# Kernel tuning notes

Measured on AMD Instinct MI355X. Metric: run time of the kernel, lower is better.

Reference implementation:

```python
import jax, jax.numpy as jnp
import numpy as np

# RosaAttention config constants
H = 16       # num_rosa_heads
KV = 4       # num_rosa_key_value_heads
QKB = 64     # num_rosa_query_key_bits
VB = 64      # num_rosa_value_bits
HID = 2048   # hidden_size
TAU = 1.0    # temperature buffer


def setup_inputs() -> dict:
    key = jax.random.key(0)
    ks = jax.random.split(key, 8)
    B, S = 2, 2048
    sc = 0.02
    return {
        "x": jax.random.normal(ks[0], (B, S, HID), jnp.float32),
        "attention_mask": jnp.ones((B, S), jnp.int32),
        "Wq": jax.random.normal(ks[1], (HID, H * QKB), jnp.float32) * sc,
        "Wk": jax.random.normal(ks[2], (HID, KV * QKB), jnp.float32) * sc,
        "Wv": jax.random.normal(ks[3], (HID, KV * VB), jnp.float32) * sc,
        "Wo": jax.random.normal(ks[4], (H * VB, HID), jnp.float32) * sc,
        "emb0": jnp.full((H, VB), -1e-05, jnp.float32),
        "emb1": jnp.full((H, VB), +1e-05, jnp.float32),
    }


def reference(x, attention_mask, Wq, Wk, Wv, Wo, emb0, emb1):
    B, S, _ = x.shape
    rep = H // KV
    # projections -> [b, s, heads, bits]
    xq = (x @ Wq).reshape(B, S, H, QKB)
    xk = (x @ Wk).reshape(B, S, KV, QKB)
    xv = (x @ Wv).reshape(B, S, KV, VB)
    # repeat_kv: each kv head repeated n_rep times contiguously
    xk = jnp.repeat(xk, rep, axis=2)   # [b, s, H, QKB]
    xv = jnp.repeat(xv, rep, axis=2)   # [b, s, H, VB]
    # soft bit quantization of q/k, tau-scaled bit-similarity score
    qb = jnp.tanh(xq)
    kb = jnp.tanh(xk)
    scores = jnp.einsum('bqhd,bkhd->bhqk', qb, kb) / (TAU * QKB)
    # causal mask + padding mask (mask True = attend)
    causal = jnp.tril(jnp.ones((S, S), bool))
    mask = causal[None, None] & attention_mask.astype(bool)[:, None, None, :]
    scores = jnp.where(mask, scores, jnp.finfo(scores.dtype).min)
    probs = jax.nn.softmax(scores, axis=-1)        # [b, h, q, k]
    # soft-binarized values: per-bit probabilities, attended, then mapped
    # through learned per-head bit embeddings emb0 (bit=0) / emb1 (bit=1)
    vp = jax.nn.sigmoid(xv)                        # [b, s, H, VB]
    ctx = jnp.einsum('bhqk,bkhv->bqhv', probs, vp) # [b, s, H, VB]
    out_bits = ctx * emb1[None, None] + (1.0 - ctx) * emb0[None, None]
    out = out_bits.reshape(B, S, H * VB) @ Wo      # [b, s, HID]
    return out
```

## Files before the change

kernel.cpp:

```cpp
#include <hip/hip_runtime.h>
#include <math.h>

typedef short bf16x8 __attribute__((ext_vector_type(8)));
typedef float f32x4 __attribute__((ext_vector_type(4)));

#define MFMA_BF16(A,B,C) __builtin_amdgcn_mfma_f32_16x16x32_bf16(A,B,C,0,0,0)

__device__ __forceinline__ unsigned short f2b(float x) {
    union { float f; unsigned int u; } v; v.f = x;
    unsigned int r = v.u + 0x7FFFu + ((v.u >> 16) & 1u);
    return (unsigned short)(r >> 16);
}

__device__ __forceinline__ void gload16(const unsigned short* g, unsigned short* l) {
    __builtin_amdgcn_global_load_lds(
        (const __attribute__((address_space(1))) unsigned int*)(g),
        (__attribute__((address_space(3))) unsigned int*)(l),
        16, 0, 0);
}

__global__ __launch_bounds__(256) void conv_bf16(const float* __restrict__ s,
                                                 unsigned short* __restrict__ d, int n)
{
    int i = blockIdx.x * blockDim.x + threadIdx.x;
    int stride = gridDim.x * blockDim.x;
    for (int idx = i * 4; idx < n; idx += stride * 4) {
        float4 v = *(const float4*)(s + idx);
        ushort4 o;
        o.x = f2b(v.x); o.y = f2b(v.y); o.z = f2b(v.z); o.w = f2b(v.w);
        *(ushort4*)(d + idx) = o;
    }
}

__global__ __launch_bounds__(256) void transp_conv_qkv(const float* __restrict__ Wq,
                                                       const float* __restrict__ Wk,
                                                       const float* __restrict__ Wv,
                                                       unsigned short* __restrict__ dst)
{
    __shared__ float t[32][33];
    const int tx = threadIdx.x, ty = threadIdx.y;
    int bx = blockIdx.x;
    const float* src; int C, cb, dco;
    if (bx < 32)      { src = Wq; C = 1024; cb = bx;      dco = 0; }
    else if (bx < 40) { src = Wk; C = 256;  cb = bx - 32; dco = 1024; }
    else              { src = Wv; C = 256;  cb = bx - 40; dco = 1280; }
    const int c = cb * 32 + tx;
    const int r0 = blockIdx.y * 32;
#pragma unroll
    for (int i = 0; i < 4; ++i)
        t[ty + i * 8][tx] = src[(size_t)(r0 + ty + i * 8) * C + c];
    __syncthreads();
    const int cc = cb * 32 + ty;
#pragma unroll
    for (int i = 0; i < 4; ++i)
        dst[(size_t)(dco + cc + i * 8) * 2048 + r0 + tx] = f2b(t[tx][ty + i * 8]);
}

__global__ __launch_bounds__(256) void transp_conv(const float* __restrict__ src, int R, int C,
                                                   unsigned short* __restrict__ dst, int pitch)
{
    __shared__ float t[32][33];
    const int tx = threadIdx.x, ty = threadIdx.y;
    const int c = blockIdx.x * 32 + tx;
    const int r0 = blockIdx.y * 32;
#pragma unroll
    for (int i = 0; i < 4; ++i)
        t[ty + i * 8][tx] = src[(size_t)(r0 + ty + i * 8) * C + c];
    __syncthreads();
    const int cc = blockIdx.x * 32 + ty;
#pragma unroll
    for (int i = 0; i < 4; ++i)
        dst[(size_t)(cc + i * 8) * pitch + r0 + tx] = f2b(t[tx][ty + i * 8]);
}

template <int MODE>
__global__ __launch_bounds__(256, 3) void gemm_bt_mfma(
    const unsigned short* __restrict__ A,
    const unsigned short* __restrict__ Bt,
    int M, int N, int K,
    float* __restrict__ Cf,
    unsigned short* __restrict__ qh,
    unsigned short* __restrict__ kh,
    unsigned short* __restrict__ vtt)
{
    __shared__ __align__(16) unsigned short As[2][2 * 128 * 32];
    __shared__ __align__(16) unsigned short Bs[2][2 * 64 * 32];

    const int tid = threadIdx.x;
    const int w = tid >> 6, lane = tid & 63, l15 = lane & 15, quad = lane >> 4;
    const int wm = w & 1, wn = w >> 1;
    const int m0 = blockIdx.y * 128, n0 = blockIdx.x * 64;

    f32x4 acc[4][2];
    const f32x4 zero4 = {0.f, 0.f, 0.f, 0.f};
#pragma unroll
    for (int i = 0; i < 4; ++i)
#pragma unroll
        for (int j = 0; j < 2; ++j) acc[i][j] = zero4;

    const int lrow = lane >> 2, lcol = (lane & 3) * 8;
    const unsigned short* AgL = A  + (size_t)(m0 + w * 32 + lrow) * K + lcol;
    const unsigned short* BgL = Bt + (size_t)(n0 + w * 16 + lrow) * K + lcol;

#pragma unroll
    for (int t = 0; t < 4; ++t) {
        const int sub = t >> 1, half = t & 1;
        gload16(AgL + (size_t)(half * 16) * K + sub * 32,
                &As[0][sub * 4096 + (w * 32 + half * 16) * 32]);
    }
#pragma unroll
    for (int kk = 0; kk < 2; ++kk)
        gload16(BgL + kk * 32, &Bs[0][kk * 2048 + (w * 16) * 32]);
    __syncthreads();

    int cb = 0;
    for (int k0 = 0; k0 < K; k0 += 64) {
        if (k0 + 64 < K) {
            const int nb = cb ^ 1;
#pragma unroll
            for (int t = 0; t < 4; ++t) {
                const int sub = t >> 1, half = t & 1;
                gload16(AgL + (size_t)(half * 16) * K + (k0 + 64) + sub * 32,
                        &As[nb][sub * 4096 + (w * 32 + half * 16) * 32]);
            }
#pragma unroll
            for (int kk = 0; kk < 2; ++kk)
                gload16(BgL + (k0 + 64) + kk * 32, &Bs[nb][kk * 2048 + (w * 16) * 32]);
        }

        bf16x8 af[4][2], bf[2][2];
#pragma unroll
        for (int kk = 0; kk < 2; ++kk) {
#pragma unroll
            for (int mt = 0; mt < 4; ++mt)
                af[mt][kk] = *(const bf16x8*)&As[cb][kk * 4096 + (wm * 64 + mt * 16 + l15) * 32 + quad * 8];
#pragma unroll
            for (int nt = 0; nt < 2; ++nt)
                bf[nt][kk] = *(const bf16x8*)&Bs[cb][kk * 2048 + (wn * 32 + nt * 16 + l15) * 32 + quad * 8];
        }
#pragma unroll
        for (int kk = 0; kk < 2; ++kk)
#pragma unroll
            for (int mt = 0; mt < 4; ++mt)
#pragma unroll
                for (int nt = 0; nt < 2; ++nt)
                    acc[mt][nt] = MFMA_BF16(af[mt][kk], bf[nt][kk], acc[mt][nt]);

        __syncthreads();
        cb ^= 1;
    }

    if (MODE == 0) {
#pragma unroll
        for (int mt = 0; mt < 4; ++mt)
#pragma unroll
            for (int nt = 0; nt < 2; ++nt) {
                const int gn = n0 + wn * 32 + nt * 16 + l15;
#pragma unroll
                for (int r = 0; r < 4; ++r) {
                    const int gm = m0 + wm * 64 + mt * 16 + quad * 4 + r;
                    Cf[(size_t)gm * N + gn] = acc[mt][nt][r];
                }
            }
    } else {
        if (n0 < 1024) {
#pragma unroll
            for (int mt = 0; mt < 4; ++mt)
#pragma unroll
                for (int nt = 0; nt < 2; ++nt) {
                    const int gn = n0 + wn * 32 + nt * 16 + l15;
#pragma unroll
                    for (int r = 0; r < 4; ++r) {
                        const int gm = m0 + wm * 64 + mt * 16 + quad * 4 + r;
                        qh[(size_t)gm * 1024 + gn] = f2b(tanhf(acc[mt][nt][r]));
                    }
                }
        } else if (n0 < 1280) {
#pragma unroll
            for (int mt = 0; mt < 4; ++mt)
#pragma unroll
                for (int nt = 0; nt < 2; ++nt) {
                    const int gn = n0 + wn * 32 + nt * 16 + l15 - 1024;
#pragma unroll
                    for (int r = 0; r < 4; ++r) {
                        const int gm = m0 + wm * 64 + mt * 16 + quad * 4 + r;
                        kh[(size_t)gm * 256 + gn] = f2b(tanhf(acc[mt][nt][r]));
                    }
                }
        } else {
#pragma unroll
            for (int mt = 0; mt < 4; ++mt)
#pragma unroll
                for (int nt = 0; nt < 2; ++nt) {
                    const int gn = n0 + wn * 32 + nt * 16 + l15 - 1280;
                    const int g = gn >> 6, vv = gn & 63;
                    const int s0 = m0 + wm * 64 + mt * 16 + quad * 4;
                    const int b = s0 >> 11, sl = s0 & 2047;
                    ushort4 pk;
                    unsigned short* pp = (unsigned short*)&pk;
#pragma unroll
                    for (int r = 0; r < 4; ++r) {
                        float sv = 1.0f / (1.0f + __expf(-acc[mt][nt][r]));
                        pp[r] = f2b(sv);
                    }
                    *(ushort4*)&vtt[((size_t)(b * 4 + g) * 64 + vv) * 2048 + sl] = pk;
                }
        }
    }
}

__global__ __launch_bounds__(256) void rosa_attn_mfma(
    const unsigned short* __restrict__ qh,
    const unsigned short* __restrict__ kh,
    const unsigned short* __restrict__ vtt,
    const int* __restrict__ amask,
    const float* __restrict__ emb0,
    const float* __restrict__ emb1,
    unsigned short* __restrict__ ob)
{
    __shared__ __align__(16) unsigned short Ks[2][64][72];
    __shared__ __align__(16) unsigned short Vs[2][64][72];
    __shared__ __align__(16) unsigned short Ps[4][16][72];
    __shared__ float Mskf[2][64];

    const int pairI = blockIdx.x;
    const int h = blockIdx.y, b = blockIdx.z, g = h >> 2;
    const int tid = threadIdx.x;
    const int w = tid >> 6, lane = tid & 63, l15 = lane & 15, quad = lane >> 4;

    const int srow0 = tid >> 3,         soff0 = (tid & 7) * 8;
    const int srow1 = (tid + 256) >> 3, soff1 = ((tid + 256) & 7) * 8;

    const unsigned short* kbase = kh + (size_t)b * 2048 * 256 + g * 64;
    const unsigned short* vbase = vtt + ((size_t)(b * 4 + g) * 64) * 2048;

    const f32x4 zero4 = {0.f, 0.f, 0.f, 0.f};
    const float cexp = 0.0225421100f;

    for (int half = 0; half < 2; ++half) {
        const int qt = (half == 0) ? pairI : 31 - pairI;
        const int q0 = qt * 64;
        const int nkt = qt + 1;
        const int qg = q0 + w * 16 + l15;

        const unsigned short* qrow = qh + ((size_t)(b * 2048 + q0 + w * 16 + l15) * 16 + h) * 64;
        const bf16x8 qf0 = *(const bf16x8*)(qrow + quad * 8);
        const bf16x8 qf1 = *(const bf16x8*)(qrow + 32 + quad * 8);

        f32x4 oacc[4];
#pragma unroll
        for (int t = 0; t < 4; ++t) oacc[t] = zero4;
        float psum = 0.0f;

        __syncthreads();
        {
            uint4 k0r = *(const uint4*)(kbase + (size_t)srow0 * 256 + soff0);
            uint4 k1r = *(const uint4*)(kbase + (size_t)srow1 * 256 + soff1);
            uint4 v0r = *(const uint4*)(vbase + (size_t)srow0 * 2048 + soff0);
            uint4 v1r = *(const uint4*)(vbase + (size_t)srow1 * 2048 + soff1);
            int mr = (tid < 64) ? amask[b * 2048 + tid] : 0;
            *(uint4*)&Ks[0][srow0][soff0] = k0r;
            *(uint4*)&Ks[0][srow1][soff1] = k1r;
            *(uint4*)&Vs[0][srow0][soff0] = v0r;
            *(uint4*)&Vs[0][srow1][soff1] = v1r;
            if (tid < 64) Mskf[0][tid] = mr ? 1.0f : 0.0f;
        }
        __syncthreads();

        int cb = 0;
        for (int kt = 0; kt < nkt; ++kt) {
            const bool haveNext = (kt + 1 < nkt);
            uint4 k0r, k1r, v0r, v1r;
            int mr = 0;
            if (haveNext) {
                const int kn = (kt + 1) * 64;
                k0r = *(const uint4*)(kbase + (size_t)(kn + srow0) * 256 + soff0);
                k1r = *(const uint4*)(kbase + (size_t)(kn + srow1) * 256 + soff1);
                v0r = *(const uint4*)(vbase + (size_t)srow0 * 2048 + kn + soff0);
                v1r = *(const uint4*)(vbase + (size_t)srow1 * 2048 + kn + soff1);
                if (tid < 64) mr = amask[b * 2048 + kn + tid];
            }

            const int k0 = kt * 64;
            const bool diag = (kt == qt);
            const int ntlim = diag ? (w + 1) : 4;

#pragma unroll
            for (int nt = 0; nt < 4; ++nt) {
                ushort4 pk;
                if (nt < ntlim) {
                    bf16x8 kf0 = *(const bf16x8*)&Ks[cb][nt * 16 + l15][quad * 8];
                    bf16x8 kf1 = *(const bf16x8*)&Ks[cb][nt * 16 + l15][32 + quad * 8];
                    f32x4 sc = MFMA_BF16(kf0, qf0, zero4);
                    sc = MFMA_BF16(kf1, qf1, sc);
                    float4 mv = *(const float4*)&Mskf[cb][nt * 16 + quad * 4];
                    const float* mvp = (const float*)&mv;
                    unsigned short* pp = (unsigned short*)&pk;
#pragma unroll
                    for (int r = 0; r < 4; ++r) {
                        float p = __builtin_exp2f(sc[r] * cexp) * mvp[r];
                        if (diag) {
                            const int jg = k0 + nt * 16 + quad * 4 + r;
                            p = (jg <= qg) ? p : 0.0f;
                        }
                        psum += p;
                        pp[r] = f2b(p);
                    }
                } else {
                    pk.x = 0; pk.y = 0; pk.z = 0; pk.w = 0;
                }
                *(ushort4*)&Ps[w][l15][nt * 16 + quad * 4] = pk;
            }

            const bf16x8 pf0 = *(const bf16x8*)&Ps[w][l15][quad * 8];
            const bf16x8 pf1 = *(const bf16x8*)&Ps[w][l15][32 + quad * 8];
#pragma unroll
            for (int nt = 0; nt < 4; ++nt) {
                bf16x8 vf0 = *(const bf16x8*)&Vs[cb][nt * 16 + l15][quad * 8];
                bf16x8 vf1 = *(const bf16x8*)&Vs[cb][nt * 16 + l15][32 + quad * 8];
                oacc[nt] = MFMA_BF16(pf0, vf0, oacc[nt]);
                oacc[nt] = MFMA_BF16(pf1, vf1, oacc[nt]);
            }

            if (haveNext) {
                const int nb = cb ^ 1;
                *(uint4*)&Ks[nb][srow0][soff0] = k0r;
                *(uint4*)&Ks[nb][srow1][soff1] = k1r;
                *(uint4*)&Vs[nb][srow0][soff0] = v0r;
                *(uint4*)&Vs[nb][srow1][soff1] = v1r;
                if (tid < 64) Mskf[nb][tid] = mr ? 1.0f : 0.0f;
                __syncthreads();
                cb = nb;
            }
        }

        float l = psum;
        l += __shfl_xor(l, 16);
        l += __shfl_xor(l, 32);
        float lq[4];
#pragma unroll
        for (int r = 0; r < 4; ++r) lq[r] = __shfl(l, quad * 4 + r);

#pragma unroll
        for (int nt = 0; nt < 4; ++nt) {
            const float e0 = emb0[h * 64 + nt * 16 + l15];
            const float e1 = emb1[h * 64 + nt * 16 + l15];
#pragma unroll
            for (int r = 0; r < 4; ++r) {
                const float ctx = oacc[nt][r] / lq[r];
                const float val = e0 + ctx * (e1 - e0);
                const size_t s_idx = (size_t)(b * 2048 + q0 + w * 16 + quad * 4 + r);
                ob[(s_idx * 16 + h) * 64 + nt * 16 + l15] = f2b(val);
            }
        }
    }
}

extern "C" void kernel_launch(void* const* d_in, const int* in_sizes, int n_in,
                              void* d_out, int out_size, void* d_ws, size_t ws_size,
                              hipStream_t stream)
{
    const float* x    = (const float*)d_in[0];
    const int*   amask= (const int*)d_in[1];
    const float* Wq   = (const float*)d_in[2];
    const float* Wk   = (const float*)d_in[3];
    const float* Wv   = (const float*)d_in[4];
    const float* Wo   = (const float*)d_in[5];
    const float* emb0 = (const float*)d_in[6];
    const float* emb1 = (const float*)d_in[7];
    float* out = (float*)d_out;

    char* base = (char*)d_ws;
    unsigned short* xh    = (unsigned short*)(base);
    unsigned short* ob    = xh;
    unsigned short* Wqkvt = (unsigned short*)(base + (16u << 20));
    unsigned short* Wot   = (unsigned short*)(base + (22u << 20));
    unsigned short* qh    = (unsigned short*)(base + (26u << 20));
    unsigned short* kh    = (unsigned short*)(base + (34u << 20));
    unsigned short* vtt   = (unsigned short*)(base + (36u << 20));

    conv_bf16<<<2048, 256, 0, stream>>>(x, xh, 4096 * 2048);
    transp_conv_qkv<<<dim3(48, 64), dim3(32, 8), 0, stream>>>(Wq, Wk, Wv, Wqkvt);
    transp_conv<<<dim3(64, 32), dim3(32, 8), 0, stream>>>(Wo, 1024, 2048, Wot, 1024);

    gemm_bt_mfma<1><<<dim3(24, 32), 256, 0, stream>>>(xh, Wqkvt, 4096, 1536, 2048,
                                                      nullptr, qh, kh, vtt);
    rosa_attn_mfma<<<dim3(16, 16, 2), 256, 0, stream>>>(qh, kh, vtt, amask, emb0, emb1, ob);
    gemm_bt_mfma<0><<<dim3(32, 32), 256, 0, stream>>>(ob, Wot, 4096, 2048, 1024,
                                                      out, nullptr, nullptr, nullptr);
}
```

Measured before the change: 238.1 us.

## Stage attention K/V tiles via direct global-to-LDS loads, one query tile per block

After: 267.6 us. 12.4% more time.

```diff
diff --git a/kernel.cpp b/kernel.cpp
--- a/kernel.cpp
+++ b/kernel.cpp
@@ -17,6 +17,12 @@
         (const __attribute__((address_space(1))) unsigned int*)(g),
         (__attribute__((address_space(3))) unsigned int*)(l),
         16, 0, 0);
+}
+__device__ __forceinline__ void gload4(const int* g, int* l) {
+    __builtin_amdgcn_global_load_lds(
+        (const __attribute__((address_space(1))) unsigned int*)(g),
+        (__attribute__((address_space(3))) unsigned int*)(l),
+        4, 0, 0);
 }
 
 __global__ __launch_bounds__(256) void conv_bf16(const float* __restrict__ s,
@@ -209,7 +215,7 @@
     }
 }
 
-__global__ __launch_bounds__(256) void rosa_attn_mfma(
+__global__ __launch_bounds__(256, 3) void rosa_attn_mfma(
     const unsigned short* __restrict__ qh,
     const unsigned short* __restrict__ kh,
     const unsigned short* __restrict__ vtt,
@@ -218,140 +224,120 @@
     const float* __restrict__ emb1,
     unsigned short* __restrict__ ob)
 {
-    __shared__ __align__(16) unsigned short Ks[2][64][72];
-    __shared__ __align__(16) unsigned short Vs[2][64][72];
+    __shared__ __align__(16) unsigned short Ks[2][2][64 * 32];
+    __shared__ __align__(16) unsigned short Vs[2][2][64 * 32];
     __shared__ __align__(16) unsigned short Ps[4][16][72];
-    __shared__ float Mskf[2][64];
-
-    const int pairI = blockIdx.x;
+    __shared__ int Mski[2][64];
+
+    const int qt = 31 - blockIdx.x;
     const int h = blockIdx.y, b = blockIdx.z, g = h >> 2;
     const int tid = threadIdx.x;
     const int w = tid >> 6, lane = tid & 63, l15 = lane & 15, quad = lane >> 4;
 
-    const int srow0 = tid >> 3,         soff0 = (tid & 7) * 8;
-    const int srow1 = (tid + 256) >> 3, soff1 = ((tid + 256) & 7) * 8;
-
+    const int q0 = qt * 64;
+    const int nkt = qt + 1;
+    const int qg = q0 + w * 16 + l15;
+
+    const int lrow = lane >> 2, lcol = (lane & 3) * 8;
     const unsigned short* kbase = kh + (size_t)b * 2048 * 256 + g * 64;
     const unsigned short* vbase = vtt + ((size_t)(b * 4 + g) * 64) * 2048;
+    const int* mbase = amask + b * 2048;
+
+    const unsigned short* qrow = qh + ((size_t)(b * 2048 + q0 + w * 16 + l15) * 16 + h) * 64;
+    const bf16x8 qf0 = *(const bf16x8*)(qrow + quad * 8);
+    const bf16x8 qf1 = *(const bf16x8*)(qrow + 32 + quad * 8);
 
     const f32x4 zero4 = {0.f, 0.f, 0.f, 0.f};
     const float cexp = 0.0225421100f;
 
-    for (int half = 0; half < 2; ++half) {
-        const int qt = (half == 0) ? pairI : 31 - pairI;
-        const int q0 = qt * 64;
-        const int nkt = qt + 1;
-        const int qg = q0 + w * 16 + l15;
-
-        const unsigned short* qrow = qh + ((size_t)(b * 2048 + q0 + w * 16 + l15) * 16 + h) * 64;
-        const bf16x8 qf0 = *(const bf16x8*)(qrow + quad * 8);
-        const bf16x8 qf1 = *(const bf16x8*)(qrow + 32 + quad * 8);
-
-        f32x4 oacc[4];
-#pragma unroll
-        for (int t = 0; t < 4; ++t) oacc[t] = zero4;
-        float psum = 0.0f;
-
-        __syncthreads();
-        {
-            uint4 k0r = *(const uint4*)(kbase + (size_t)srow0 * 256 + soff0);
-            uint4 k1r = *(const uint4*)(kbase + (size_t)srow1 * 256 + soff1);
-            uint4 v0r = *(const uint4*)(vbase + (size_t)srow0 * 2048 + soff0);
-            uint4 v1r = *(const uint4*)(vbase + (size_t)srow1 * 2048 + soff1);
-            int mr = (tid < 64) ? amask[b * 2048 + tid] : 0;
-            *(uint4*)&Ks[0][srow0][soff0] = k0r;
-            *(uint4*)&Ks[0][srow1][soff1] = k1r;
-            *(uint4*)&Vs[0][srow0][soff0] = v0r;
-            *(uint4*)&Vs[0][srow1][soff1] = v1r;
-            if (tid < 64) Mskf[0][tid] = mr ? 1.0f : 0.0f;
-        }
-        __syncthreads();
-
-        int cb = 0;
-        for (int kt = 0; kt < nkt; ++kt) {
-            const bool haveNext = (kt + 1 < nkt);
-            uint4 k0r, k1r, v0r, v1r;
-            int mr = 0;
-            if (haveNext) {
-                const int kn = (kt + 1) * 64;
-                k0r = *(const uint4*)(kbase + (size_t)(kn + srow0) * 256 + soff0);
-                k1r = *(const uint4*)(kbase + (size_t)(kn + srow1) * 256 + soff1);
-                v0r = *(const uint4*)(vbase + (size_t)srow0 * 2048 + kn + soff0);
-                v1r = *(const uint4*)(vbase + (size_t)srow1 * 2048 + kn + soff1);
-                if (tid < 64) mr = amask[b * 2048 + kn + tid];
+    f32x4 oacc[4];
+#pragma unroll
+    for (int t = 0; t < 4; ++t) oacc[t] = zero4;
+    float psum = 0.0f;
+
+#define STAGE_TILE(k0s, buf)                                                          \
+    {                                                                                 \
+        _Pragma("unroll")                                                             \
+        for (int kk = 0; kk < 2; ++kk) {                                              \
+            gload16(kbase + (size_t)((k0s) + w * 16 + lrow) * 256 + kk * 32 + lcol,   \
+                    &Ks[buf][kk][(w * 16) * 32]);                                     \
+            gload16(vbase + (size_t)(w * 16 + lrow) * 2048 + (k0s) + kk * 32 + lcol,  \
+                    &Vs[buf][kk][(w * 16) * 32]);                                     \
+        }                                                                             \
+        if (w == 0) gload4(mbase + (k0s) + lane, &Mski[buf][0]);                      \
+    }
+
+    STAGE_TILE(0, 0)
+    __syncthreads();
+
+    int cb = 0;
+    for (int kt = 0; kt < nkt; ++kt) {
+        if (kt + 1 < nkt) STAGE_TILE((kt + 1) * 64, cb ^ 1)
+
+        const int k0 = kt * 64;
+        const bool diag = (kt == qt);
+        const int ntlim = diag ? (w + 1) : 4;
+
+#pragma unroll
+        for (int nt = 0; nt < 4; ++nt) {
+            ushort4 pk;
+            if (nt < ntlim) {
+                bf16x8 kf0 = *(const bf16x8*)&Ks[cb][0][(nt * 16 + l15) * 32 + quad * 8];
+                bf16x8 kf1 = *(const bf16x8*)&Ks[cb][1][(nt * 16 + l15) * 32 + quad * 8];
+                f32x4 sc = MFMA_BF16(kf0, qf0, zero4);
+                sc = MFMA_BF16(kf1, qf1, sc);
+                const int4 m4 = *(const int4*)&Mski[cb][nt * 16 + quad * 4];
+                const int* mm = (const int*)&m4;
+                unsigned short* pp = (unsigned short*)&pk;
+#pragma unroll
+                for (int r = 0; r < 4; ++r) {
+                    float p = __builtin_exp2f(sc[r] * cexp);
+                    bool valid = (mm[r] != 0);
+                    if (diag) valid = valid && ((k0 + nt * 16 + quad * 4 + r) <= qg);
+                    p = valid ? p : 0.0f;
+                    psum += p;
+                    pp[r] = f2b(p);
+                }
+            } else {
+                pk.x = 0; pk.y = 0; pk.z = 0; pk.w = 0;
             }
-
-            const int k0 = kt * 64;
-            const bool diag = (kt == qt);
-            const int ntlim = diag ? (w + 1) : 4;
-
-#pragma unroll
-            for (int nt = 0; nt < 4; ++nt) {
-                ushort4 pk;
-                if (nt < ntlim) {
-                    bf16x8 kf0 = *(const bf16x8*)&Ks[cb][nt * 16 + l15][quad * 8];
-                    bf16x8 kf1 = *(const bf16x8*)&Ks[cb][nt * 16 + l15][32 + quad * 8];
-                    f32x4 sc = MFMA_BF16(kf0, qf0, zero4);
-                    sc = MFMA_BF16(kf1, qf1, sc);
-                    float4 mv = *(const float4*)&Mskf[cb][nt * 16 + quad * 4];
-                    const float* mvp = (const float*)&mv;
-                    unsigned short* pp = (unsigned short*)&pk;
-#pragma unroll
-                    for (int r = 0; r < 4; ++r) {
-                        float p = __builtin_exp2f(sc[r] * cexp) * mvp[r];
-                        if (diag) {
-                            const int jg = k0 + nt * 16 + quad * 4 + r;
-                            p = (jg <= qg) ? p : 0.0f;
-                        }
-                        psum += p;
-                        pp[r] = f2b(p);
-                    }
-                } else {
-                    pk.x = 0; pk.y = 0; pk.z = 0; pk.w = 0;
-                }
-                *(ushort4*)&Ps[w][l15][nt * 16 + quad * 4] = pk;
-            }
-
-            const bf16x8 pf0 = *(const bf16x8*)&Ps[w][l15][quad * 8];
-            const bf16x8 pf1 = *(const bf16x8*)&Ps[w][l15][32 + quad * 8];
-#pragma unroll
-            for (int nt = 0; nt < 4; ++nt) {
-                bf16x8 vf0 = *(const bf16x8*)&Vs[cb][nt * 16 + l15][quad * 8];
-                bf16x8 vf1 = *(const bf16x8*)&Vs[cb][nt * 16 + l15][32 + quad * 8];
-                oacc[nt] = MFMA_BF16(pf0, vf0, oacc[nt]);
-                oacc[nt] = MFMA_BF16(pf1, vf1, oacc[nt]);
-            }
-
-            if (haveNext) {
-                const int nb = cb ^ 1;
-                *(uint4*)&Ks[nb][srow0][soff0] = k0r;
-                *(uint4*)&Ks[nb][srow1][soff1] = k1r;
-                *(uint4*)&Vs[nb][srow0][soff0] = v0r;
-                *(uint4*)&Vs[nb][srow1][soff1] = v1r;
-                if (tid < 64) Mskf[nb][tid] = mr ? 1.0f : 0.0f;
-                __syncthreads();
-                cb = nb;
-            }
-        }
-
-        float l = psum;
-        l += __shfl_xor(l, 16);
-        l += __shfl_xor(l, 32);
-        float lq[4];
-#pragma unroll
-        for (int r = 0; r < 4; ++r) lq[r] = __shfl(l, quad * 4 + r);
-
+            *(ushort4*)&Ps[w][l15][nt * 16 + quad * 4] = pk;
+        }
+
+        const bf16x8 pf0 = *(const bf16x8*)&Ps[w][l15][quad * 8];
+        const bf16x8 pf1 = *(const bf16x8*)&Ps[w][l15][32 + quad * 8];
 #pragma unroll
         for (int nt = 0; nt < 4; ++nt) {
-            const float e0 = emb0[h * 64 + nt * 16 + l15];
-            const float e1 = emb1[h * 64 + nt * 16 + l15];
-#pragma unroll
-            for (int r = 0; r < 4; ++r) {
-                const float ctx = oacc[nt][r] / lq[r];
-                const float val = e0 + ctx * (e1 - e0);
-                const size_t s_idx = (size_t)(b * 2048 + q0 + w * 16 + quad * 4 + r);
-                ob[(s_idx * 16 + h) * 64 + nt * 16 + l15] = f2b(val);
-            }
+            bf16x8 vf0 = *(const bf16x8*)&Vs[cb][0][(nt * 16 + l15) * 32 + quad * 8];
+            bf16x8 vf1 = *(const bf16x8*)&Vs[cb][1][(nt * 16 + l15) * 32 + quad * 8];
+            oacc[nt] = MFMA_BF16(pf0, vf0, oacc[nt]);
+            oacc[nt] = MFMA_BF16(pf1, vf1, oacc[nt]);
+        }
+
+        if (kt + 1 < nkt) {
+            __syncthreads();
+            cb ^= 1;
+        }
+    }
+#undef STAGE_TILE
+
+    float l = psum;
+    l += __shfl_xor(l, 16);
+    l += __shfl_xor(l, 32);
+    float lq[4];
+#pragma unroll
+    for (int r = 0; r < 4; ++r) lq[r] = __shfl(l, quad * 4 + r);
+
+#pragma unroll
+    for (int nt = 0; nt < 4; ++nt) {
+        const float e0 = emb0[h * 64 + nt * 16 + l15];
+        const float e1 = emb1[h * 64 + nt * 16 + l15];
+#pragma unroll
+        for (int r = 0; r < 4; ++r) {
+            const float ctx = oacc[nt][r] / lq[r];
+            const float val = e0 + ctx * (e1 - e0);
+            const size_t s_idx = (size_t)(b * 2048 + q0 + w * 16 + quad * 4 + r);
+            ob[(s_idx * 16 + h) * 64 + nt * 16 + l15] = f2b(val);
         }
     }
 }
@@ -385,7 +371,7 @@
 
     gemm_bt_mfma<1><<<dim3(24, 32), 256, 0, stream>>>(xh, Wqkvt, 4096, 1536, 2048,
                                                       nullptr, qh, kh, vtt);
-    rosa_attn_mfma<<<dim3(16, 16, 2), 256, 0, stream>>>(qh, kh, vtt, amask, emb0, emb1, ob);
+    rosa_attn_mfma<<<dim3(32, 16, 2), 256, 0, stream>>>(qh, kh, vtt, amask, emb0, emb1, ob);
     gemm_bt_mfma<0><<<dim3(32, 32), 256, 0, stream>>>(ob, Wot, 4096, 2048, 1024,
                                                       out, nullptr, nullptr, nullptr);
 }
```
